# Kernel optimization log

Measured on AMD Instinct MI355X. Metric: run time of the kernel, lower is better.

Reference implementation:

```python
import jax, jax.numpy as jnp
import numpy as np
import math

N = 131072        # number of query points
IN_DIM = 3
G = 5             # grid_level = num_sin_layers - 2
F = 8             # feature_dims per level
W = 256           # hidden width (ffenc_dims[1:])
OUT = 64          # num_outputs
BOUND = 1.0
BASE_SIGMA = 1.0
EXP_SIGMA = 2.0
SIN_W0 = 5.0      # multires - 1 = n_levels - 1


def setup_inputs() -> dict:
    key = jax.random.key(0)
    ks = jax.random.split(key, 9)
    in_pos = jax.random.uniform(ks[0], (N, IN_DIM), jnp.float32, -BOUND, BOUND)
    grid_feats = jax.random.normal(ks[1], (N, G * F), jnp.float32) * 0.01  # grid_embed_std
    ffn_A = jax.random.normal(ks[2], (G, F, W), jnp.float32)
    # SIREN-style inits (scaled normals approximating uniform SIREN init ranges)
    W0 = jax.random.normal(ks[3], (IN_DIM, W), jnp.float32) / IN_DIM
    b0 = jax.random.normal(ks[4], (W,), jnp.float32) * 0.01
    Wh = jax.random.normal(ks[5], (G, W, W), jnp.float32) * (math.sqrt(6.0 / W) / SIN_W0)
    bh = jax.random.normal(ks[6], (G, W), jnp.float32) * 0.01
    Wh_high = jax.random.normal(ks[7], (G, W, OUT), jnp.float32) * (math.sqrt(6.0 / W) / SIN_W0)
    bh_high = jax.random.normal(ks[8], (G, OUT), jnp.float32) * 0.01
    return {"in_pos": in_pos, "grid_feats": grid_feats, "ffn_A": ffn_A,
            "W0": W0, "b0": b0, "Wh": Wh, "bh": bh,
            "Wh_high": Wh_high, "bh_high": bh_high}


def reference(in_pos, grid_feats, ffn_A, W0, b0, Wh, bh, Wh_high, bh_high):
    sigmas = BASE_SIGMA * (EXP_SIGMA ** jnp.arange(G, dtype=jnp.float32))  # [G]
    embed = lambda h: jnp.sin(SIN_W0 * h)  # dim-preserving periodic embedding

    x = in_pos / BOUND                                   # [N, 3]
    # grid branch: per-level Fourier projection of hash-grid features
    gx = jnp.transpose(grid_feats.reshape(-1, G, F), (1, 0, 2))  # [G, N, F]
    ffn = ffn_A * sigmas[:, None, None]                   # [G, F, W]
    gx = jnp.sin((2.0 * math.pi) * jnp.einsum('gnf,gfw->gnw', gx, ffn))  # [G, N, W]

    # SIREN branch, layer 0
    x = embed(x @ W0 + b0)                                # [N, W]
    x_out = jnp.zeros((x.shape[0], OUT), dtype=x.dtype)
    for l in range(G):  # layers 1 .. num_sin_layers-2
        x = embed(x @ Wh[l] + bh[l])                      # [N, W]
        x = gx[l] + x                                     # grid residual
        x_out = x_out + embed(x @ Wh_high[l] + bh_high[l])
    return x_out
```

## Files before the change

### kernel.cpp

```cpp
#include <hip/hip_runtime.h>


#define TM 64
#define XSTRIDE 264
#define GSTRIDE 48
#define K5 0.79577471545947667f

typedef __attribute__((ext_vector_type(8))) _Float16 v8h;
typedef __attribute__((ext_vector_type(2))) __fp16 hw2;
typedef __attribute__((ext_vector_type(4))) float v4f;
typedef __attribute__((ext_vector_type(16))) float v16f;

#define MFMA16H(a, b, c) __builtin_amdgcn_mfma_f32_16x16x32_f16(a, b, c, 0, 0, 0)
#define MFMA32H(a, b, c) __builtin_amdgcn_mfma_f32_32x32x16_f16(a, b, c, 0, 0, 0)

__device__ __forceinline__ float sin_rev(float u) {
#if __has_builtin(__builtin_amdgcn_fractf)
    return __builtin_amdgcn_sinf(__builtin_amdgcn_fractf(u));
#else
    return __builtin_amdgcn_sinf(u - floorf(u));
#endif
}

__device__ __forceinline__ short f16s(float x) {
    _Float16 hh = (_Float16)x;
    return __builtin_bit_cast(short, hh);
}

__global__ __launch_bounds__(256) void ffb_pack(
    const float* __restrict__ Wh, const float* __restrict__ Whh,
    const float* __restrict__ ffnA,
    short* __restrict__ wh, short* __restrict__ whh, short* __restrict__ gf)
{
    int t = blockIdx.x * 256 + threadIdx.x;
    if (t < 40960) {
        int lane = t & 63, nt = (t >> 6) & 7, kb = (t >> 9) & 15, l = t >> 13;
        int n = nt * 32 + (lane & 31);
        int k0 = kb * 16 + (lane >> 5) * 8;
        short hs[8];
        #pragma unroll
        for (int jj = 0; jj < 8; jj++)
            hs[jj] = f16s(Wh[(l * 256 + k0 + jj) * 256 + n] * K5);
        *(v8h*)(wh + t * 8) = *(v8h*)hs;
    } else if (t < 51200) {
        int t2 = t - 40960;
        int lane = t2 & 63, nt = (t2 >> 6) & 3, kb = (t2 >> 8) & 7, l = t2 >> 11;
        int n = nt * 16 + (lane & 15);
        int k0 = kb * 32 + (lane >> 4) * 8;
        short hs[8];
        #pragma unroll
        for (int jj = 0; jj < 8; jj++)
            hs[jj] = f16s(Whh[(l * 256 + k0 + jj) * 64 + n] * K5);
        *(v8h*)(whh + t2 * 8) = *(v8h*)hs;
    } else if (t < 53760) {
        int t3 = t - 51200;
        int lane = t3 & 63, nt = (t3 >> 6) & 7, l = t3 >> 9;
        int n = nt * 32 + (lane & 31);
        const float sc = 0.5f * (float)(1 << l);
        short hs[8];
        #pragma unroll
        for (int jj = 0; jj < 8; jj++)
            hs[jj] = f16s(ffnA[(l * 8 + jj) * 256 + n] * sc);
        *(v8h*)(gf + t3 * 8) = *(v8h*)hs;
    }
}

__global__ __launch_bounds__(256, 3) void ffb_main(
    const float* __restrict__ pos, const float* __restrict__ gfeat,
    const float* __restrict__ W0, const float* __restrict__ b0,
    const float* __restrict__ bh, const float* __restrict__ bhh,
    const short* __restrict__ wh, const short* __restrict__ whh,
    const short* __restrict__ gf,
    float* __restrict__ out)
{
    __shared__ __align__(16) short s_x[TM * XSTRIDE];
    __shared__ __align__(16) short s_g[TM * GSTRIDE];
    __shared__ float s_pos[TM * 3];

    const int tid = threadIdx.x;
    const int row0 = blockIdx.x * TM;
    const int lane = tid & 63;
    const int w = tid >> 6;
    const int i = lane & 15;
    const int q = lane >> 4;
    const int m32 = lane & 31;
    const int h = lane >> 5;

    if (tid < TM * 3) s_pos[tid] = pos[row0 * 3 + tid];
    for (int k2 = tid; k2 < TM * 40; k2 += 256) {
        int r = k2 / 40, f = k2 % 40;
        s_g[r * GSTRIDE + f] = f16s(gfeat[row0 * 40 + k2]);
    }
    __syncthreads();

    {
        const int c = tid;
        const float w00 = W0[c], w01 = W0[256 + c], w02 = W0[512 + c], bc = b0[c];
        #pragma unroll 4
        for (int r = 0; r < TM; r++) {
            float d = s_pos[r * 3 + 0] * w00 + s_pos[r * 3 + 1] * w01
                    + s_pos[r * 3 + 2] * w02 + bc;
            s_x[r * XSTRIDE + c] = f16s(sin_rev(d * K5));
        }
    }
    __syncthreads();

    float cout[4][4];
    #pragma unroll
    for (int m = 0; m < 4; m++)
        #pragma unroll
        for (int r = 0; r < 4; r++) cout[m][r] = 0.f;

    const int a1off0 = m32 * XSTRIDE + h * 8;
    const int a1off1 = (32 + m32) * XSTRIDE + h * 8;

    for (int l = 0; l < 5; l++) {
        const float bias0 = bh[l * 256 + w * 64 + m32] * K5;
        const float bias1 = bh[l * 256 + w * 64 + 32 + m32] * K5;
        v16f C1[2][2];
        #pragma unroll
        for (int r = 0; r < 16; r++) {
            C1[0][0][r] = bias0; C1[1][0][r] = bias0;
            C1[0][1][r] = bias1; C1[1][1][r] = bias1;
        }
        v8h gb0 = *(const v8h*)(gf + ((l * 8 + w * 2 + 0) * 64 + lane) * 8);
        v8h gb1 = *(const v8h*)(gf + ((l * 8 + w * 2 + 1) * 64 + lane) * 8);

        {
            const short* bp = wh + l * 65536 + (2 * w) * 512 + lane * 8;
            v8h rb0[4], rb1[4];
            #pragma unroll
            for (int p = 0; p < 3; p++) {
                rb0[p] = *(const v8h*)(bp + p * 4096);
                rb1[p] = *(const v8h*)(bp + p * 4096 + 512);
            }
            #pragma unroll
            for (int kb = 0; kb < 16; kb++) {
                if (kb + 3 < 16) {
                    rb0[(kb + 3) & 3] = *(const v8h*)(bp + (kb + 3) * 4096);
                    rb1[(kb + 3) & 3] = *(const v8h*)(bp + (kb + 3) * 4096 + 512);
                }
                v8h a0 = *(const v8h*)&s_x[a1off0 + kb * 16];
                v8h a1 = *(const v8h*)&s_x[a1off1 + kb * 16];
                v8h bc0 = rb0[kb & 3], bc1 = rb1[kb & 3];
                C1[0][0] = MFMA32H(a0, bc0, C1[0][0]);
                C1[0][1] = MFMA32H(a0, bc1, C1[0][1]);
                C1[1][0] = MFMA32H(a1, bc0, C1[1][0]);
                C1[1][1] = MFMA32H(a1, bc1, C1[1][1]);
            }
        }
        __syncthreads();

        #pragma unroll
        for (int m = 0; m < 2; m++) {
            v8h ga = *(const v8h*)&s_g[(m * 32 + m32) * GSTRIDE + l * 8];
            #pragma unroll
            for (int t = 0; t < 2; t++) {
                v16f Z = {};
                v16f G = MFMA32H(ga, (t ? gb1 : gb0), Z);
                const int col = w * 64 + t * 32 + m32;
                #pragma unroll
                for (int r = 0; r < 16; r++) {
                    const int row = m * 32 + (r & 3) + 8 * (r >> 2) + 4 * h;
                    float v = sin_rev(C1[m][t][r]) + sin_rev(G[r]);
                    s_x[row * XSTRIDE + col] = f16s(v);
                }
            }
        }
        __syncthreads();

        const float b2 = bhh[l * 64 + w * 16 + i] * K5;
        v4f C2[4];
        #pragma unroll
        for (int m = 0; m < 4; m++) C2[m] = (v4f){b2, b2, b2, b2};
        {
            const short* bp = whh + l * 16384 + w * 512 + lane * 8;
            v8h bc[8];
            #pragma unroll
            for (int kb = 0; kb < 8; kb++)
                bc[kb] = *(const v8h*)(bp + kb * 2048);
            #pragma unroll
            for (int kb = 0; kb < 8; kb++) {
                #pragma unroll
                for (int m = 0; m < 4; m++) {
                    v8h a = *(const v8h*)&s_x[(m * 16 + i) * XSTRIDE + q * 8 + kb * 32];
                    C2[m] = MFMA16H(a, bc[kb], C2[m]);
                }
            }
        }
        #pragma unroll
        for (int m = 0; m < 4; m++)
            #pragma unroll
            for (int r = 0; r < 4; r++)
                cout[m][r] += sin_rev(C2[m][r]);
    }

    #pragma unroll
    for (int m = 0; m < 4; m++)
        #pragma unroll
        for (int r = 0; r < 4; r++)
            out[(row0 + m * 16 + q * 4 + r) * 64 + w * 16 + i] = cout[m][r];
}

extern "C" void kernel_launch(void* const* d_in, const int* in_sizes, int n_in,
                              void* d_out, int out_size, void* d_ws, size_t ws_size,
                              hipStream_t stream) {
    const float* pos   = (const float*)d_in[0];
    const float* gfeat = (const float*)d_in[1];
    const float* ffnA  = (const float*)d_in[2];
    const float* W0    = (const float*)d_in[3];
    const float* b0    = (const float*)d_in[4];
    const float* Wh    = (const float*)d_in[5];
    const float* bh    = (const float*)d_in[6];
    const float* Whh   = (const float*)d_in[7];
    const float* bhh   = (const float*)d_in[8];
    float* out = (float*)d_out;
    const int N = in_sizes[0] / 3;

    short* wh  = (short*)d_ws;
    short* whh = wh + 327680;
    short* gf  = whh + 81920;

    ffb_pack<<<210, 256, 0, stream>>>(Wh, Whh, ffnA, wh, whh, gf);
    ffb_main<<<N / TM, 256, 0, stream>>>(pos, gfeat, W0, b0, bh, bhh,
                                         wh, whh, gf, out);
}
```

Measured before the change: 231.6 us.

## Transpose MFMA operands for vectorized LDS stores and use 32x32 MFMA for output layer

```diff
diff --git a/kernel.cpp b/kernel.cpp
--- a/kernel.cpp
+++ b/kernel.cpp
@@ -7,11 +7,10 @@
 #define K5 0.79577471545947667f
 
 typedef __attribute__((ext_vector_type(8))) _Float16 v8h;
-typedef __attribute__((ext_vector_type(2))) __fp16 hw2;
+typedef __attribute__((ext_vector_type(4))) _Float16 v4h;
 typedef __attribute__((ext_vector_type(4))) float v4f;
 typedef __attribute__((ext_vector_type(16))) float v16f;
 
-#define MFMA16H(a, b, c) __builtin_amdgcn_mfma_f32_16x16x32_f16(a, b, c, 0, 0, 0)
 #define MFMA32H(a, b, c) __builtin_amdgcn_mfma_f32_32x32x16_f16(a, b, c, 0, 0, 0)
 
 __device__ __forceinline__ float sin_rev(float u) {
@@ -30,7 +29,9 @@
 __global__ __launch_bounds__(256) void ffb_pack(
     const float* __restrict__ Wh, const float* __restrict__ Whh,
     const float* __restrict__ ffnA,
-    short* __restrict__ wh, short* __restrict__ whh, short* __restrict__ gf)
+    const float* __restrict__ bh, const float* __restrict__ bhh,
+    short* __restrict__ wh, short* __restrict__ whh, short* __restrict__ gf,
+    float* __restrict__ bhs, float* __restrict__ bhhs)
 {
     int t = blockIdx.x * 256 + threadIdx.x;
     if (t < 40960) {
@@ -44,9 +45,9 @@
         *(v8h*)(wh + t * 8) = *(v8h*)hs;
     } else if (t < 51200) {
         int t2 = t - 40960;
-        int lane = t2 & 63, nt = (t2 >> 6) & 3, kb = (t2 >> 8) & 7, l = t2 >> 11;
-        int n = nt * 16 + (lane & 15);
-        int k0 = kb * 32 + (lane >> 4) * 8;
+        int lane = t2 & 63, nt = (t2 >> 6) & 1, kb = (t2 >> 7) & 15, l = t2 >> 11;
+        int n = nt * 32 + (lane & 31);
+        int k0 = kb * 16 + (lane >> 5) * 8;
         short hs[8];
         #pragma unroll
         for (int jj = 0; jj < 8; jj++)
@@ -62,13 +63,19 @@
         for (int jj = 0; jj < 8; jj++)
             hs[jj] = f16s(ffnA[(l * 8 + jj) * 256 + n] * sc);
         *(v8h*)(gf + t3 * 8) = *(v8h*)hs;
+    } else if (t < 55040) {
+        int t4 = t - 53760;
+        bhs[t4] = bh[t4] * K5;
+    } else if (t < 55360) {
+        int t5 = t - 55040;
+        bhhs[t5] = bhh[t5] * K5;
     }
 }
 
 __global__ __launch_bounds__(256, 3) void ffb_main(
     const float* __restrict__ pos, const float* __restrict__ gfeat,
     const float* __restrict__ W0, const float* __restrict__ b0,
-    const float* __restrict__ bh, const float* __restrict__ bhh,
+    const float* __restrict__ bhs, const float* __restrict__ bhhs,
     const short* __restrict__ wh, const short* __restrict__ whh,
     const short* __restrict__ gf,
     float* __restrict__ out)
@@ -81,10 +88,10 @@
     const int row0 = blockIdx.x * TM;
     const int lane = tid & 63;
     const int w = tid >> 6;
-    const int i = lane & 15;
-    const int q = lane >> 4;
     const int m32 = lane & 31;
     const int h = lane >> 5;
+    const int mq = w >> 1;
+    const int tq = w & 1;
 
     if (tid < TM * 3) s_pos[tid] = pos[row0 * 3 + tid];
     for (int k2 = tid; k2 < TM * 40; k2 += 256) {
@@ -105,23 +112,28 @@
     }
     __syncthreads();
 
-    float cout[4][4];
+    float cout[16];
     #pragma unroll
-    for (int m = 0; m < 4; m++)
-        #pragma unroll
-        for (int r = 0; r < 4; r++) cout[m][r] = 0.f;
+    for (int r = 0; r < 16; r++) cout[r] = 0.f;
 
     const int a1off0 = m32 * XSTRIDE + h * 8;
     const int a1off1 = (32 + m32) * XSTRIDE + h * 8;
 
     for (int l = 0; l < 5; l++) {
-        const float bias0 = bh[l * 256 + w * 64 + m32] * K5;
-        const float bias1 = bh[l * 256 + w * 64 + 32 + m32] * K5;
         v16f C1[2][2];
-        #pragma unroll
-        for (int r = 0; r < 16; r++) {
-            C1[0][0][r] = bias0; C1[1][0][r] = bias0;
-            C1[0][1][r] = bias1; C1[1][1][r] = bias1;
+        {
+            const float* bl = bhs + l * 256 + w * 64 + h * 4;
+            #pragma unroll
+            for (int tt = 0; tt < 2; tt++)
+                #pragma unroll
+                for (int rq = 0; rq < 4; rq++) {
+                    v4f b = *(const v4f*)(bl + tt * 32 + rq * 8);
+                    #pragma unroll
+                    for (int j = 0; j < 4; j++) {
+                        C1[0][tt][rq * 4 + j] = b[j];
+                        C1[1][tt][rq * 4 + j] = b[j];
+                    }
+                }
         }
         v8h gb0 = *(const v8h*)(gf + ((l * 8 + w * 2 + 0) * 64 + lane) * 8);
         v8h gb1 = *(const v8h*)(gf + ((l * 8 + w * 2 + 1) * 64 + lane) * 8);
@@ -143,10 +155,10 @@
                 v8h a0 = *(const v8h*)&s_x[a1off0 + kb * 16];
                 v8h a1 = *(const v8h*)&s_x[a1off1 + kb * 16];
                 v8h bc0 = rb0[kb & 3], bc1 = rb1[kb & 3];
-                C1[0][0] = MFMA32H(a0, bc0, C1[0][0]);
-                C1[0][1] = MFMA32H(a0, bc1, C1[0][1]);
-                C1[1][0] = MFMA32H(a1, bc0, C1[1][0]);
-                C1[1][1] = MFMA32H(a1, bc1, C1[1][1]);
+                C1[0][0] = MFMA32H(bc0, a0, C1[0][0]);
+                C1[0][1] = MFMA32H(bc1, a0, C1[0][1]);
+                C1[1][0] = MFMA32H(bc0, a1, C1[1][0]);
+                C1[1][1] = MFMA32H(bc1, a1, C1[1][1]);
             }
         }
         __syncthreads();
@@ -154,52 +166,51 @@
         #pragma unroll
         for (int m = 0; m < 2; m++) {
             v8h ga = *(const v8h*)&s_g[(m * 32 + m32) * GSTRIDE + l * 8];
-            #pragma unroll
-            for (int t = 0; t < 2; t++) {
+            const int rowb = (m * 32 + m32) * XSTRIDE;
+            #pragma unroll
+            for (int tt = 0; tt < 2; tt++) {
                 v16f Z = {};
-                v16f G = MFMA32H(ga, (t ? gb1 : gb0), Z);
-                const int col = w * 64 + t * 32 + m32;
+                v16f G = MFMA32H((tt ? gb1 : gb0), ga, Z);
+                const int cb = rowb + w * 64 + tt * 32 + h * 4;
                 #pragma unroll
-                for (int r = 0; r < 16; r++) {
-                    const int row = m * 32 + (r & 3) + 8 * (r >> 2) + 4 * h;
-                    float v = sin_rev(C1[m][t][r]) + sin_rev(G[r]);
-                    s_x[row * XSTRIDE + col] = f16s(v);
+                for (int rq = 0; rq < 4; rq++) {
+                    v4h pv;
+                    #pragma unroll
+                    for (int j = 0; j < 4; j++)
+                        pv[j] = (_Float16)(sin_rev(C1[m][tt][rq * 4 + j])
+                                         + sin_rev(G[rq * 4 + j]));
+                    *(v4h*)(s_x + cb + rq * 8) = pv;
                 }
             }
         }
         __syncthreads();
 
-        const float b2 = bhh[l * 64 + w * 16 + i] * K5;
-        v4f C2[4];
-        #pragma unroll
-        for (int m = 0; m < 4; m++) C2[m] = (v4f){b2, b2, b2, b2};
         {
-            const short* bp = whh + l * 16384 + w * 512 + lane * 8;
-            v8h bc[8];
-            #pragma unroll
-            for (int kb = 0; kb < 8; kb++)
-                bc[kb] = *(const v8h*)(bp + kb * 2048);
-            #pragma unroll
-            for (int kb = 0; kb < 8; kb++) {
-                #pragma unroll
-                for (int m = 0; m < 4; m++) {
-                    v8h a = *(const v8h*)&s_x[(m * 16 + i) * XSTRIDE + q * 8 + kb * 32];
-                    C2[m] = MFMA16H(a, bc[kb], C2[m]);
-                }
-            }
-        }
-        #pragma unroll
-        for (int m = 0; m < 4; m++)
-            #pragma unroll
-            for (int r = 0; r < 4; r++)
-                cout[m][r] += sin_rev(C2[m][r]);
+            const float b2 = bhhs[l * 64 + tq * 32 + m32];
+            v16f C2;
+            #pragma unroll
+            for (int r = 0; r < 16; r++) C2[r] = b2;
+            const short* bp2 = whh + l * 16384 + tq * 512 + lane * 8;
+            v8h bc[16];
+            #pragma unroll
+            for (int kb = 0; kb < 16; kb++)
+                bc[kb] = *(const v8h*)(bp2 + kb * 1024);
+            const int aoff = mq ? a1off1 : a1off0;
+            #pragma unroll
+            for (int kb = 0; kb < 16; kb++) {
+                v8h a = *(const v8h*)&s_x[aoff + kb * 16];
+                C2 = MFMA32H(a, bc[kb], C2);
+            }
+            #pragma unroll
+            for (int r = 0; r < 16; r++) cout[r] += sin_rev(C2[r]);
+        }
     }
 
     #pragma unroll
-    for (int m = 0; m < 4; m++)
-        #pragma unroll
-        for (int r = 0; r < 4; r++)
-            out[(row0 + m * 16 + q * 4 + r) * 64 + w * 16 + i] = cout[m][r];
+    for (int r = 0; r < 16; r++) {
+        const int orow = row0 + mq * 32 + (r & 3) + 8 * (r >> 2) + 4 * h;
+        out[orow * 64 + tq * 32 + m32] = cout[r];
+    }
 }
 
 extern "C" void kernel_launch(void* const* d_in, const int* in_sizes, int n_in,
@@ -220,8 +231,11 @@
     short* wh  = (short*)d_ws;
     short* whh = wh + 327680;
     short* gf  = whh + 81920;
-
-    ffb_pack<<<210, 256, 0, stream>>>(Wh, Whh, ffnA, wh, whh, gf);
-    ffb_main<<<N / TM, 256, 0, stream>>>(pos, gfeat, W0, b0, bh, bhh,
+    float* bhs  = (float*)(gf + 20480);
+    float* bhhs = bhs + 1280;
+
+    ffb_pack<<<217, 256, 0, stream>>>(Wh, Whh, ffnA, bh, bhh,
+                                      wh, whh, gf, bhs, bhhs);
+    ffb_main<<<N / TM, 256, 0, stream>>>(pos, gfeat, W0, b0, bhs, bhhs,
                                          wh, whh, gf, out);
 }
```

Result: no change. 232.3 us (+0.3%).
